# Optimization experiments

Measured on AMD Instinct MI355X. Metric: run time of the kernel, lower is better.

Reference implementation:

```python
import jax, jax.numpy as jnp
import numpy as np

TEMPERATURE = 0.1
NUM_CLASSES = 100
BATCH = 4096
DIM = 128


def setup_inputs() -> dict:
    key = jax.random.key(0)
    k1, k2, k3 = jax.random.split(key, 3)
    centers1 = jax.random.normal(k1, (NUM_CLASSES, DIM), dtype=jnp.float32)
    features = jax.random.normal(k2, (BATCH, 2, DIM), dtype=jnp.float32)
    # contrastive features are typically L2-normalized; harmless and realistic
    centers1 = centers1 / jnp.linalg.norm(centers1, axis=-1, keepdims=True)
    features = features / jnp.linalg.norm(features, axis=-1, keepdims=True)
    targets = jax.random.randint(k3, (BATCH,), 0, NUM_CLASSES, dtype=jnp.int64 if jax.config.jax_enable_x64 else jnp.int32)
    return {"centers1": centers1, "features": features, "targets": targets}


def reference(centers1, features, targets):
    C = centers1.shape[0]          # num classes
    B = features.shape[0]          # batch size
    t = TEMPERATURE

    # targets for [view0; view1; class centers] -> [2B + C]
    tgt = jnp.concatenate([targets, targets, jnp.arange(C, dtype=targets.dtype)])
    # per-class count over all 2B+C target entries (eye(C)[targets].sum(0))
    batch_cls_count = jnp.zeros((C,), jnp.float32).at[tgt].add(1.0)

    # positive mask [2B, 2B+C], zero out self-contrast on the diagonal
    mask = (tgt[: 2 * B, None] == tgt[None, :]).astype(jnp.float32)
    idx = jnp.arange(2 * B)
    logits_mask = jnp.ones((2 * B, 2 * B + C), jnp.float32).at[idx, idx].set(0.0)
    mask = mask * logits_mask

    # stack: [view0 (B), view1 (B), centers (C)] -> [2B+C, D]
    feats = jnp.concatenate([features[:, 0], features[:, 1], centers1], axis=0)

    # logits [2B, 2B+C], stable max-subtract (detached max)
    logits = jnp.matmul(feats[: 2 * B], feats.T) / t
    logits = logits - jax.lax.stop_gradient(jnp.max(logits, axis=1, keepdims=True))

    exp_logits = jnp.exp(logits) * logits_mask
    # per-instance class-balanced weight, minus mask (as in original)
    per_ins_weight = batch_cls_count[tgt][None, :] - mask  # [2B, 2B+C] via broadcast
    exp_logits_sum = jnp.sum(exp_logits / per_ins_weight, axis=1, keepdims=True)

    log_prob = logits - jnp.log(exp_logits_sum)
    mean_log_prob_pos = jnp.sum(mask * log_prob, axis=1) / jnp.sum(mask, axis=1)
    loss = -mean_log_prob_pos
    return loss.reshape(2, B).mean()
```

## Files before the change

kernel.cpp:

```cpp
#include <hip/hip_runtime.h>
#include <math.h>

constexpr int B_   = 4096;
constexpr int C_   = 100;
constexpr int D_   = 128;
constexpr int TWOB = 8192;
constexpr int NJ   = 8292;
constexpr int NJP  = 8320;
constexpr float LOG2E10 = 14.4269504089f;

typedef __attribute__((ext_vector_type(8))) short short8;
typedef __attribute__((ext_vector_type(4))) float f32x4;


__device__ __forceinline__ const float* feat_row(const float* __restrict__ centers,
                                                 const float* __restrict__ features,
                                                 int idx) {
  if (idx < B_)   return features + (size_t)idx * (2 * D_);
  if (idx < TWOB) return features + (size_t)(idx - B_) * (2 * D_) + D_;
  return centers + (size_t)(idx - TWOB) * D_;
}

__device__ __forceinline__ unsigned short f2bf(float x) {
  unsigned int u = __float_as_uint(x);
  unsigned int r = (u + 0x7FFFu + ((u >> 16) & 1u)) >> 16;
  return (unsigned short)r;
}

__device__ __forceinline__ float bf2f(short s) {
  return __uint_as_float(((unsigned int)(unsigned short)s) << 16);
}

__global__ void count_kernel(const int* __restrict__ targets, int* __restrict__ cnt) {
  int i = blockIdx.x * 256 + threadIdx.x;
  if (i < B_) atomicAdd(&cnt[targets[i]], 1);
}

__global__ __launch_bounds__(256)
void prep_kernel(const float* __restrict__ centers, const float* __restrict__ features,
                 const int* __restrict__ targets, const int* __restrict__ cnt,
                 unsigned short* __restrict__ fbB, unsigned short* __restrict__ fbA,
                 float4* __restrict__ tbl, float* __restrict__ G) {
  int gidx = blockIdx.x * 256 + threadIdx.x;
  if (gidx >= NJP * 32) return;
  int row = gidx >> 5;
  int q   = gidx & 31;
  float4 v = make_float4(0.f, 0.f, 0.f, 0.f);
  int jt = -9;
  if (row < NJ) {
    v  = *(const float4*)(feat_row(centers, features, row) + q * 4);
    jt = (row < B_) ? targets[row] : (row < TWOB ? targets[row - B_] : row - TWOB);
  }
  ushort4 o;
  o.x = f2bf(v.x); o.y = f2bf(v.y); o.z = f2bf(v.z); o.w = f2bf(v.w);
  *(ushort4*)&fbB[(size_t)row * 128 + q * 4] = o;
  if (row < TWOB) {
    ushort4 a;
    a.x = f2bf(v.x * LOG2E10); a.y = f2bf(v.y * LOG2E10);
    a.z = f2bf(v.z * LOG2E10); a.w = f2bf(v.w * LOG2E10);
    *(ushort4*)&fbA[(size_t)row * 128 + q * 4] = a;
  }
  if (row < NJ) {
    float* gc = G + jt * 128 + q * 4;
    atomicAdd(gc + 0, bf2f((short)o.x));
    atomicAdd(gc + 1, bf2f((short)o.y));
    atomicAdd(gc + 2, bf2f((short)o.z));
    atomicAdd(gc + 3, bf2f((short)o.w));
  }
  if (q == 0) {
    float r0 = 0.f, r1 = 0.f;
    if (jt >= 0) {
      float b = (float)(2 * cnt[jt] + 1);
      r0 = 1.f / b;
      r1 = 1.f / (b - 1.f);
    }
    tbl[row] = make_float4(__int_as_float(jt), r0, r1, 0.f);
  }
}

__global__ __launch_bounds__(256, 2)
void bal_mfma(const unsigned short* __restrict__ fbA, const unsigned short* __restrict__ fbB,
              const float4* __restrict__ tbl, float* __restrict__ Eacc) {
  const int t     = threadIdx.x;
  const int lane  = t & 63;
  const int w     = t >> 6;
  const int id    = blockIdx.x;
  const int strip = id & 15;
  const int isup  = id >> 4;
  const int rbase = isup * 256 + w * 64;
  const int lr    = lane & 15;
  const int lh    = lane >> 4;

  const int jg0 = strip * 16 + (strip < 4 ? strip : 4);
  const int jg1 = jg0 + 16 + (strip < 4 ? 1 : 0);

  short8 af[4][4];
  #pragma unroll
  for (int ks = 0; ks < 4; ++ks)
    #pragma unroll
    for (int m = 0; m < 4; ++m)
      af[ks][m] = *(const short8*)&fbA[(size_t)(rbase + m * 16 + lr) * 128 + (ks * 4 + lh) * 8];

  int ti[4][4];
  #pragma unroll
  for (int m = 0; m < 4; ++m)
    #pragma unroll
    for (int g = 0; g < 4; ++g)
      ti[m][g] = __float_as_int(tbl[rbase + m * 16 + lh * 4 + g].x);

  float ep[4][4];
  #pragma unroll
  for (int m = 0; m < 4; ++m)
    #pragma unroll
    for (int g = 0; g < 4; ++g) ep[m][g] = 0.f;

  short8 b0[2][4], b1[2][4];
  float4 t0[2], t1[2];

  auto loadB = [&](int jg, short8 (&b)[2][4], float4 (&tb)[2]) {
    int jb = jg * 32;
    #pragma unroll
    for (int n = 0; n < 2; ++n) {
      tb[n] = tbl[jb + n * 16 + lr];
      #pragma unroll
      for (int ks = 0; ks < 4; ++ks)
        b[n][ks] = *(const short8*)&fbB[(size_t)(jb + n * 16 + lr) * 128 + (ks * 4 + lh) * 8];
    }
  };

  auto compute = [&](short8 (&b)[2][4], float4 (&tb)[2]) {
    f32x4 acc[4][2];
    #pragma unroll
    for (int m = 0; m < 4; ++m)
      #pragma unroll
      for (int n = 0; n < 2; ++n) acc[m][n] = (f32x4){0.f, 0.f, 0.f, 0.f};
    #pragma unroll
    for (int ks = 0; ks < 4; ++ks)
      #pragma unroll
      for (int n = 0; n < 2; ++n)
        #pragma unroll
        for (int m = 0; m < 4; ++m)
          acc[m][n] = __builtin_amdgcn_mfma_f32_16x16x32_bf16(af[ks][m], b[n][ks], acc[m][n], 0, 0, 0);
    #pragma unroll
    for (int n = 0; n < 2; ++n) {
      int   jtn = __float_as_int(tb[n].x);
      float r0  = tb[n].y, r1 = tb[n].z;
      #pragma unroll
      for (int m = 0; m < 4; ++m)
        #pragma unroll
        for (int g = 0; g < 4; ++g) {
          float e = __builtin_amdgcn_exp2f(acc[m][n][g]);
          ep[m][g] = fmaf(e, (ti[m][g] == jtn) ? r1 : r0, ep[m][g]);
        }
    }
  };

  int jg = jg0;
  loadB(jg0, b0, t0);
  while (jg + 2 <= jg1) {
    loadB(jg + 1, b1, t1);
    compute(b0, t0);
    if (jg + 2 < jg1) loadB(jg + 2, b0, t0);
    compute(b1, t1);
    jg += 2;
  }
  if (jg < jg1) compute(b0, t0);

  #pragma unroll
  for (int mk = 1; mk <= 8; mk <<= 1)
    #pragma unroll
    for (int m = 0; m < 4; ++m)
      #pragma unroll
      for (int g = 0; g < 4; ++g)
        ep[m][g] += __shfl_xor(ep[m][g], mk, 64);
  if (lr == 0) {
    #pragma unroll
    for (int m = 0; m < 4; ++m)
      #pragma unroll
      for (int g = 0; g < 4; ++g)
        atomicAdd(&Eacc[rbase + m * 16 + lh * 4 + g], ep[m][g]);
  }
}

__global__ __launch_bounds__(256)
void bal_final(const unsigned short* __restrict__ fbA, const unsigned short* __restrict__ fbB,
               const float4* __restrict__ tbl, const float* __restrict__ G,
               const float* __restrict__ Eacc, float* __restrict__ out) {
  int t    = threadIdx.x;
  int row  = blockIdx.x * 64 + (t >> 2);
  int part = t & 3;
  const unsigned short* pa = fbA + (size_t)row * 128 + part * 32;
  const unsigned short* pb = fbB + (size_t)row * 128 + part * 32;
  float4 tb = tbl[row];
  int   ti  = __float_as_int(tb.x);
  const float* gp = G + ti * 128 + part * 32;

  float sA = 0.f, sB = 0.f, sG = 0.f;
  #pragma unroll
  for (int q = 0; q < 4; ++q) {
    short8 va = *(const short8*)&pa[q * 8];
    short8 vb = *(const short8*)&pb[q * 8];
    #pragma unroll
    for (int d = 0; d < 8; ++d) {
      float fa = bf2f(va[d]);
      float fb = bf2f(vb[d]);
      float gv = gp[q * 8 + d];
      sA = fmaf(fa, fb, sA);
      sB = fmaf(fb, fb, sB);
      sG = fmaf(fb, gv, sG);
    }
  }
  sA += __shfl_xor(sA, 1, 64); sA += __shfl_xor(sA, 2, 64);
  sB += __shfl_xor(sB, 1, 64); sB += __shfl_xor(sB, 2, 64);
  sG += __shfl_xor(sG, 1, 64); sG += __shfl_xor(sG, 2, 64);

  float r1 = tb.z;
  float ep = Eacc[row] - __builtin_amdgcn_exp2f(sA) * r1;
  float ma = 10.f * (sG - sB);
  float li = ma * r1 - logf(ep);
  float local = -li * (1.f / (8192.f * 4.f));

  #pragma unroll
  for (int mk = 1; mk < 64; mk <<= 1) local += __shfl_xor(local, mk, 64);
  if ((t & 63) == 0) atomicAdd(out, local);
}

extern "C" void kernel_launch(void* const* d_in, const int* in_sizes, int n_in,
                              void* d_out, int out_size, void* d_ws, size_t ws_size,
                              hipStream_t stream) {
  const float* centers  = (const float*)d_in[0];
  const float* features = (const float*)d_in[1];
  const int*   targets  = (const int*)d_in[2];

  char* ws = (char*)d_ws;
  int*            cnt  = (int*)ws;
  float*          Eacc = (float*)(ws + 512);
  float*          G    = (float*)(ws + 33280);
  float4*         tbl  = (float4*)(ws + 84480);
  unsigned short* fbB  = (unsigned short*)(ws + 217600);
  unsigned short* fbA  = (unsigned short*)(ws + 2347520);
  float* out = (float*)d_out;

  hipMemsetAsync(ws, 0, 84480, stream);
  hipMemsetAsync(d_out, 0, sizeof(float), stream);
  count_kernel<<<(B_ + 255) / 256, 256, 0, stream>>>(targets, cnt);
  prep_kernel<<<(NJP * 32 + 255) / 256, 256, 0, stream>>>(centers, features, targets, cnt,
                                                          fbB, fbA, tbl, G);
  bal_mfma<<<512, 256, 0, stream>>>(fbA, fbB, tbl, Eacc);
  bal_final<<<TWOB / 64, 256, 0, stream>>>(fbA, fbB, tbl, G, Eacc, out);
}
```

Measured before the change: 141.6 us.

## Replace per-element atomic class-sum with dedicated per-class gather reduction kernel

The per-class feature sum G was accumulated with about a million float atomics inside the prep kernel, which are heavily contended because there are only 100 classes. A new gsum kernel instead launches one block per class and row chunk; each block scans a precomputed target array and accumulates that class's rows in registers, then issues a single atomic per dimension. The count kernel now also writes a combined target table that the other kernels read. In exchange each gsum block walks about a thousand rows serially, reading the targets redundantly across 100 classes, and there is one more launch. The mfma kernel's occupancy hint also moves from launch bounds to waves_per_eu.

```diff
diff --git a/kernel.cpp b/kernel.cpp
--- a/kernel.cpp
+++ b/kernel.cpp
@@ -31,26 +31,28 @@
   return __uint_as_float(((unsigned int)(unsigned short)s) << 16);
 }
 
-__global__ void count_kernel(const int* __restrict__ targets, int* __restrict__ cnt) {
+__global__ __launch_bounds__(256)
+void tgt_count_kernel(const int* __restrict__ targets, int* __restrict__ cnt,
+                      int* __restrict__ tgtAll) {
   int i = blockIdx.x * 256 + threadIdx.x;
-  if (i < B_) atomicAdd(&cnt[targets[i]], 1);
+  if (i >= NJP) return;
+  int jt = (i < B_) ? targets[i]
+         : (i < TWOB ? targets[i - B_] : (i < NJ ? i - TWOB : -9));
+  tgtAll[i] = jt;
+  if (i < B_) atomicAdd(&cnt[jt], 1);
 }
 
 __global__ __launch_bounds__(256)
 void prep_kernel(const float* __restrict__ centers, const float* __restrict__ features,
-                 const int* __restrict__ targets, const int* __restrict__ cnt,
+                 const int* __restrict__ tgtAll, const int* __restrict__ cnt,
                  unsigned short* __restrict__ fbB, unsigned short* __restrict__ fbA,
-                 float4* __restrict__ tbl, float* __restrict__ G) {
+                 float4* __restrict__ tbl) {
   int gidx = blockIdx.x * 256 + threadIdx.x;
   if (gidx >= NJP * 32) return;
   int row = gidx >> 5;
   int q   = gidx & 31;
   float4 v = make_float4(0.f, 0.f, 0.f, 0.f);
-  int jt = -9;
-  if (row < NJ) {
-    v  = *(const float4*)(feat_row(centers, features, row) + q * 4);
-    jt = (row < B_) ? targets[row] : (row < TWOB ? targets[row - B_] : row - TWOB);
-  }
+  if (row < NJ) v = *(const float4*)(feat_row(centers, features, row) + q * 4);
   ushort4 o;
   o.x = f2bf(v.x); o.y = f2bf(v.y); o.z = f2bf(v.z); o.w = f2bf(v.w);
   *(ushort4*)&fbB[(size_t)row * 128 + q * 4] = o;
@@ -60,14 +62,8 @@
     a.z = f2bf(v.z * LOG2E10); a.w = f2bf(v.w * LOG2E10);
     *(ushort4*)&fbA[(size_t)row * 128 + q * 4] = a;
   }
-  if (row < NJ) {
-    float* gc = G + jt * 128 + q * 4;
-    atomicAdd(gc + 0, bf2f((short)o.x));
-    atomicAdd(gc + 1, bf2f((short)o.y));
-    atomicAdd(gc + 2, bf2f((short)o.z));
-    atomicAdd(gc + 3, bf2f((short)o.w));
-  }
   if (q == 0) {
+    int jt = tgtAll[row];
     float r0 = 0.f, r1 = 0.f;
     if (jt >= 0) {
       float b = (float)(2 * cnt[jt] + 1);
@@ -78,7 +74,25 @@
   }
 }
 
-__global__ __launch_bounds__(256, 2)
+__global__ __launch_bounds__(128)
+void gsum_kernel(const float* __restrict__ centers, const float* __restrict__ features,
+                 const int* __restrict__ tgtAll, float* __restrict__ G) {
+  const int c     = blockIdx.x;
+  const int chunk = blockIdx.y;
+  const int d     = threadIdx.x;
+  int r0 = chunk * 1037;
+  int r1 = r0 + 1037; if (r1 > NJ) r1 = NJ;
+  float acc = 0.f;
+  for (int r = r0; r < r1; ++r) {
+    if (tgtAll[r] == c) {
+      float v = feat_row(centers, features, r)[d];
+      acc += bf2f((short)f2bf(v));
+    }
+  }
+  if (acc != 0.f) atomicAdd(&G[c * 128 + d], acc);
+}
+
+__global__ __launch_bounds__(256) __attribute__((amdgpu_waves_per_eu(2, 2)))
 void bal_mfma(const unsigned short* __restrict__ fbA, const unsigned short* __restrict__ fbB,
               const float4* __restrict__ tbl, float* __restrict__ Eacc) {
   const int t     = threadIdx.x;
@@ -233,19 +247,21 @@
   const int*   targets  = (const int*)d_in[2];
 
   char* ws = (char*)d_ws;
-  int*            cnt  = (int*)ws;
-  float*          Eacc = (float*)(ws + 512);
-  float*          G    = (float*)(ws + 33280);
-  float4*         tbl  = (float4*)(ws + 84480);
-  unsigned short* fbB  = (unsigned short*)(ws + 217600);
-  unsigned short* fbA  = (unsigned short*)(ws + 2347520);
+  int*            cnt    = (int*)ws;
+  float*          Eacc   = (float*)(ws + 512);
+  float*          G      = (float*)(ws + 33280);
+  int*            tgtAll = (int*)(ws + 84480);
+  float4*         tbl    = (float4*)(ws + 117760);
+  unsigned short* fbB    = (unsigned short*)(ws + 250880);
+  unsigned short* fbA    = (unsigned short*)(ws + 2380800);
   float* out = (float*)d_out;
 
   hipMemsetAsync(ws, 0, 84480, stream);
   hipMemsetAsync(d_out, 0, sizeof(float), stream);
-  count_kernel<<<(B_ + 255) / 256, 256, 0, stream>>>(targets, cnt);
-  prep_kernel<<<(NJP * 32 + 255) / 256, 256, 0, stream>>>(centers, features, targets, cnt,
-                                                          fbB, fbA, tbl, G);
+  tgt_count_kernel<<<(NJP + 255) / 256, 256, 0, stream>>>(targets, cnt, tgtAll);
+  prep_kernel<<<(NJP * 32 + 255) / 256, 256, 0, stream>>>(centers, features, tgtAll, cnt,
+                                                          fbB, fbA, tbl);
+  gsum_kernel<<<dim3(C_, 8), 128, 0, stream>>>(centers, features, tgtAll, G);
   bal_mfma<<<512, 256, 0, stream>>>(fbA, fbB, tbl, Eacc);
   bal_final<<<TWOB / 64, 256, 0, stream>>>(fbA, fbB, tbl, G, Eacc, out);
 }
```

Result: slower. 181.7 us (+28.3%).
